# Kernel tuning notes

Hardware: AMD Instinct MI355X
Metric: run time of the kernel (lower is better)

The kernel has to match this reference:

```python
import jax, jax.numpy as jnp
import numpy as np

N_NODES = 150018  # n_users + n_items + n_genres
LATENT_DIM = 64
N_LAYERS = 3
N_EDGES = 4_800_000


def setup_inputs() -> dict:
    key = jax.random.key(0)
    k1, k2, k3, k4 = jax.random.split(key, 4)
    embedding = jax.random.normal(k1, (N_NODES, LATENT_DIM), dtype=jnp.float32) * 0.01
    vals = jax.random.uniform(k2, (N_EDGES,), dtype=jnp.float32)
    rows = jax.random.randint(k3, (N_EDGES,), 0, N_NODES, dtype=jnp.int32)
    cols = jax.random.randint(k4, (N_EDGES,), 0, N_NODES, dtype=jnp.int32)
    return {"embedding": embedding, "vals": vals, "rows": rows, "cols": cols}


def _spmm(vals, rows, cols, x):
    # sparse.mm(adj, x): out[r] += vals[e] * x[cols[e]] for each edge e
    gathered = x[cols] * vals[:, None]  # [E, D]
    return jax.ops.segment_sum(gathered, rows, num_segments=N_NODES)


def reference(embedding, vals, rows, cols):
    # LightGCN-style propagation; dropout is identity in eval mode (training=False)
    emb = embedding
    acc = emb
    for _ in range(N_LAYERS):
        emb = _spmm(vals, rows, cols, emb)
        acc = acc + emb
    # mean over (n_layers + 1) stacked layer outputs
    return acc / jnp.asarray(N_LAYERS + 1, dtype=embedding.dtype)
```

## Files before the change

### kernel.cpp

```cpp
#include <hip/hip_runtime.h>

#define N_NODES 150018
#define DIMS 64
#define NELEM (N_NODES * DIMS)
#define NVEC4 (NELEM / 4)
#define NBKT ((N_NODES + 255) >> 8)
#define BCAP 9216
#define PADCAP 1792
#define BSTRIDE (BCAP + PADCAP)
#define CH 8192
#define EPP 8
#define VINV 6.10388817e-05f

__device__ __forceinline__ unsigned short f2bf(float f) {
    unsigned int u = __float_as_uint(f);
    u += 0x7FFFu + ((u >> 16) & 1u);
    return (unsigned short)(u >> 16);
}
__device__ __forceinline__ float bf2f(unsigned short h) {
    return __uint_as_float(((unsigned int)h) << 16);
}

__global__ void conv_bf16_k(const float4* __restrict__ src, ushort4* __restrict__ dst, int n4) {
    int i = blockIdx.x * blockDim.x + threadIdx.x;
    if (i < n4) {
        float4 v = src[i];
        dst[i] = make_ushort4(f2bf(v.x), f2bf(v.y), f2bf(v.z), f2bf(v.w));
    }
}

__global__ void init_cursor_k(int* __restrict__ cursor) {
    int i = blockIdx.x * blockDim.x + threadIdx.x;
    if (i < NBKT) cursor[i] = i * BCAP;
}

__global__ __launch_bounds__(1024) void scatter_bucket_k(const int* __restrict__ rows,
                                 const int* __restrict__ cols,
                                 const float* __restrict__ vals, int* __restrict__ cursor,
                                 int2* __restrict__ edges1, int n) {
    __shared__ int2 staged[CH];
    __shared__ int cnt[NBKT];
    __shared__ int base[NBKT];
    __shared__ int lofs[NBKT];
    __shared__ int s[1024];
    const int t = threadIdx.x;
    const int beg = blockIdx.x * CH;
    const int end = min(n, beg + CH);
    const int cn = end - beg;

    for (int i = t; i < NBKT; i += 1024) cnt[i] = 0;
    __syncthreads();

    int er[EPP], ec[EPP];
    float ev[EPP];
    #pragma unroll
    for (int k = 0; k < EPP; ++k) {
        int e = beg + t + (k << 10);
        if (e < end) {
            er[k] = rows[e]; ec[k] = cols[e]; ev[k] = vals[e];
            atomicAdd(&cnt[er[k] >> 8], 1);
        } else er[k] = -1;
    }
    __syncthreads();

    for (int i = t; i < NBKT; i += 1024) {
        int c = cnt[i];
        base[i] = c ? atomicAdd(&cursor[i], c) : 0;
    }
    int v = (t < NBKT) ? cnt[t] : 0;
    s[t] = v;
    __syncthreads();
    for (int off = 1; off < 1024; off <<= 1) {
        int tv = (t >= off) ? s[t - off] : 0;
        __syncthreads();
        s[t] += tv;
        __syncthreads();
    }
    if (t < NBKT) { lofs[t] = s[t] - v; cnt[t] = 0; }
    __syncthreads();

    #pragma unroll
    for (int k = 0; k < EPP; ++k) {
        if (er[k] >= 0) {
            int b = er[k] >> 8;
            int p = lofs[b] + atomicAdd(&cnt[b], 1);
            unsigned int q = (unsigned int)(ev[k] * 16383.0f + 0.5f);
            staged[p] = make_int2(ec[k] | ((er[k] & 255) << 18),
                                  (int)(q | ((unsigned int)b << 14)));
        }
    }
    __syncthreads();

    for (int i = t; i < cn; i += 1024) {
        int2 st = staged[i];
        int b = ((unsigned int)st.y) >> 14;
        int gpos = base[b] + i - lofs[b];
        edges1[gpos] = make_int2(st.x, st.y & 0x3FFF);
    }
}

__global__ __launch_bounds__(512) void sort_bucket_k(const int2* __restrict__ e1,
                                 const int* __restrict__ bucket_end,
                                 unsigned int* __restrict__ e2,
                                 int* __restrict__ row_offs) {
    __shared__ int cnt[256];
    __shared__ int pref[256];
    __shared__ int rank[256];
    int b = blockIdx.x;
    int beg = b * BCAP, end = bucket_end[b];
    int padbase = b * BSTRIDE;
    if (threadIdx.x < 256) cnt[threadIdx.x] = 0;
    __syncthreads();
    for (int e = beg + threadIdx.x; e < end; e += 512)
        atomicAdd(&cnt[e1[e].x >> 18], 1);
    __syncthreads();
    int pc = 0;
    if (threadIdx.x < 256) {
        pc = (cnt[threadIdx.x] + 7) & ~7;
        pref[threadIdx.x] = pc;
    }
    __syncthreads();
    for (int off = 1; off < 256; off <<= 1) {
        int t = (threadIdx.x >= off && threadIdx.x < 256) ? pref[threadIdx.x - off] : 0;
        __syncthreads();
        if (threadIdx.x < 256) pref[threadIdx.x] += t;
        __syncthreads();
    }
    if (threadIdx.x < 256) {
        int ex = pref[threadIdx.x] - pc;
        row_offs[b * 257 + threadIdx.x] = padbase + ex;
        if (threadIdx.x == 255) row_offs[b * 257 + 256] = padbase + pref[255];
        pref[threadIdx.x] = ex;
        rank[threadIdx.x] = 0;
        int fb = padbase + ex + cnt[threadIdx.x];
        int fe = padbase + ex + pc;
        for (int i = fb; i < fe; ++i) e2[i] = 0u;
    }
    __syncthreads();
    for (int e = beg + threadIdx.x; e < end; e += 512) {
        int2 ed = e1[e];
        int slot = ed.x >> 18;
        int pos = padbase + pref[slot] + atomicAdd(&rank[slot], 1);
        e2[pos] = (unsigned int)(ed.x & 0x3FFFF) | (((unsigned int)ed.y) << 18);
    }
}

__global__ __launch_bounds__(256) void spmm_mid_k(const ushort4* __restrict__ xb,
                          const unsigned int* __restrict__ edges,
                          const int* __restrict__ row_offs,
                          ushort4* __restrict__ buf_out, int n_rows) {
    int row = (blockIdx.x * blockDim.x + threadIdx.x) >> 6;
    if (row >= n_rows) return;
    int lane = threadIdx.x & 63;
    int g = lane >> 4, q = lane & 15;
    int oi = (row >> 8) * 257 + (row & 255);
    int beg = row_offs[oi], end = row_offs[oi + 1];
    float4 a0 = make_float4(0.f, 0.f, 0.f, 0.f);
    float4 a1 = make_float4(0.f, 0.f, 0.f, 0.f);
    for (int e = beg; e < end; e += 8) {
        unsigned int w0 = edges[e + g];
        unsigned int w1 = edges[e + g + 4];
        ushort4 x0 = xb[((w0 & 0x3FFFFu) << 4) + q];
        ushort4 x1 = xb[((w1 & 0x3FFFFu) << 4) + q];
        float v0 = (float)(w0 >> 18) * VINV;
        float v1 = (float)(w1 >> 18) * VINV;
        a0.x = fmaf(v0, bf2f(x0.x), a0.x);  a0.y = fmaf(v0, bf2f(x0.y), a0.y);
        a0.z = fmaf(v0, bf2f(x0.z), a0.z);  a0.w = fmaf(v0, bf2f(x0.w), a0.w);
        a1.x = fmaf(v1, bf2f(x1.x), a1.x);  a1.y = fmaf(v1, bf2f(x1.y), a1.y);
        a1.z = fmaf(v1, bf2f(x1.z), a1.z);  a1.w = fmaf(v1, bf2f(x1.w), a1.w);
    }
    float4 a = make_float4(a0.x + a1.x, a0.y + a1.y, a0.z + a1.z, a0.w + a1.w);
    #pragma unroll
    for (int m = 16; m <= 32; m <<= 1) {
        a.x += __shfl_xor(a.x, m, 64);
        a.y += __shfl_xor(a.y, m, 64);
        a.z += __shfl_xor(a.z, m, 64);
        a.w += __shfl_xor(a.w, m, 64);
    }
    if (g == 0)
        buf_out[(row << 4) + q] = make_ushort4(f2bf(a.x), f2bf(a.y), f2bf(a.z), f2bf(a.w));
}

__global__ __launch_bounds__(256) void spmm_final_k(const ushort4* __restrict__ xb,
                          const unsigned int* __restrict__ edges,
                          const int* __restrict__ row_offs,
                          const ushort4* __restrict__ embb,
                          const ushort4* __restrict__ bufA,
                          const ushort4* __restrict__ bufB,
                          float4* __restrict__ out, int n_rows) {
    int row = (blockIdx.x * blockDim.x + threadIdx.x) >> 6;
    if (row >= n_rows) return;
    int lane = threadIdx.x & 63;
    int g = lane >> 4, q = lane & 15;
    int o = (row << 4) + q;

    ushort4 em = make_ushort4(0, 0, 0, 0);
    ushort4 ra = make_ushort4(0, 0, 0, 0), rb = make_ushort4(0, 0, 0, 0);
    if (g == 1) { em = embb[o]; ra = bufA[o]; rb = bufB[o]; }

    int oi = (row >> 8) * 257 + (row & 255);
    int beg = row_offs[oi], end = row_offs[oi + 1];
    float4 a0 = make_float4(0.f, 0.f, 0.f, 0.f);
    float4 a1 = make_float4(0.f, 0.f, 0.f, 0.f);
    for (int e = beg; e < end; e += 8) {
        unsigned int w0 = edges[e + g];
        unsigned int w1 = edges[e + g + 4];
        ushort4 x0 = xb[((w0 & 0x3FFFFu) << 4) + q];
        ushort4 x1 = xb[((w1 & 0x3FFFFu) << 4) + q];
        float v0 = (float)(w0 >> 18) * VINV;
        float v1 = (float)(w1 >> 18) * VINV;
        a0.x = fmaf(v0, bf2f(x0.x), a0.x);  a0.y = fmaf(v0, bf2f(x0.y), a0.y);
        a0.z = fmaf(v0, bf2f(x0.z), a0.z);  a0.w = fmaf(v0, bf2f(x0.w), a0.w);
        a1.x = fmaf(v1, bf2f(x1.x), a1.x);  a1.y = fmaf(v1, bf2f(x1.y), a1.y);
        a1.z = fmaf(v1, bf2f(x1.z), a1.z);  a1.w = fmaf(v1, bf2f(x1.w), a1.w);
    }
    float4 a = make_float4(a0.x + a1.x, a0.y + a1.y, a0.z + a1.z, a0.w + a1.w);
    #pragma unroll
    for (int m = 16; m <= 32; m <<= 1) {
        a.x += __shfl_xor(a.x, m, 64);
        a.y += __shfl_xor(a.y, m, 64);
        a.z += __shfl_xor(a.z, m, 64);
        a.w += __shfl_xor(a.w, m, 64);
    }
    if (g == 1) {
        float4 r;
        r.x = (bf2f(em.x) + bf2f(ra.x) + bf2f(rb.x) + a.x) * 0.25f;
        r.y = (bf2f(em.y) + bf2f(ra.y) + bf2f(rb.y) + a.y) * 0.25f;
        r.z = (bf2f(em.z) + bf2f(ra.z) + bf2f(rb.z) + a.z) * 0.25f;
        r.w = (bf2f(em.w) + bf2f(ra.w) + bf2f(rb.w) + a.w) * 0.25f;
        out[o] = r;
    }
}

extern "C" void kernel_launch(void* const* d_in, const int* in_sizes, int n_in,
                              void* d_out, int out_size, void* d_ws, size_t ws_size,
                              hipStream_t stream) {
    const float* emb  = (const float*)d_in[0];
    const float* vals = (const float*)d_in[1];
    const int*   rows = (const int*)d_in[2];
    const int*   cols = (const int*)d_in[3];
    float*       out  = (float*)d_out;
    const int n_edges = in_sizes[1];

    char* w = (char*)d_ws;
    int2*   edges1 = (int2*)w;
    ushort* bufAb  = (ushort*)w;
    ushort* bufBb  = (ushort*)(w + (size_t)NELEM * 2);
    w += (size_t)NBKT * BCAP * 8;
    unsigned int* edges2 = (unsigned int*)w;
    w += (size_t)NBKT * BSTRIDE * 4;
    ushort* embb   = (ushort*)w; w += (size_t)NELEM * 2;
    int* cursor    = (int*)w;    w += (size_t)NBKT * 4;
    int* row_offs  = (int*)w;

    const int scb = (n_edges + CH - 1) / CH;

    init_cursor_k<<<1, 1024, 0, stream>>>(cursor);
    scatter_bucket_k<<<scb, 1024, 0, stream>>>(rows, cols, vals, cursor, edges1, n_edges);
    sort_bucket_k<<<NBKT, 512, 0, stream>>>(edges1, cursor, edges2, row_offs);
    conv_bf16_k<<<(NVEC4 + 255) / 256, 256, 0, stream>>>((const float4*)emb,
                                                         (ushort4*)embb, NVEC4);

    const int sp_grid = (N_NODES + 3) / 4;
    spmm_mid_k<<<sp_grid, 256, 0, stream>>>((const ushort4*)embb, edges2, row_offs,
                                            (ushort4*)bufAb, N_NODES);
    spmm_mid_k<<<sp_grid, 256, 0, stream>>>((const ushort4*)bufAb, edges2, row_offs,
                                            (ushort4*)bufBb, N_NODES);
    spmm_final_k<<<sp_grid, 256, 0, stream>>>((const ushort4*)bufBb, edges2, row_offs,
                                              (const ushort4*)embb, (const ushort4*)bufAb,
                                              (const ushort4*)bufBb, (float4*)out, N_NODES);
}
```

Baseline: 378.3 us.

## Sub-sort edges within each row by column bin and stage bucket in LDS

The bucket sort now keys each edge on its row slot plus a 16-way column bin, so edges inside a row are grouped by column range. The intent is better cache locality for the x[col] gathers in the SpMM kernels. The bucket's edges are also staged in shared memory (about 74KB for the staged array and 32KB for the counters), so the second pass no longer rereads them from global memory. The larger LDS footprint lowers occupancy of the sort kernel, and the extra counting adds work there.

```diff
diff --git a/kernel.cpp b/kernel.cpp
--- a/kernel.cpp
+++ b/kernel.cpp
@@ -103,20 +103,29 @@
                                  const int* __restrict__ bucket_end,
                                  unsigned int* __restrict__ e2,
                                  int* __restrict__ row_offs) {
-    __shared__ int cnt[256];
+    __shared__ int2 staged[BCAP];
+    __shared__ int cnt[4096];
+    __shared__ int binoff[4096];
     __shared__ int pref[256];
-    __shared__ int rank[256];
     int b = blockIdx.x;
     int beg = b * BCAP, end = bucket_end[b];
+    int n = end - beg;
     int padbase = b * BSTRIDE;
-    if (threadIdx.x < 256) cnt[threadIdx.x] = 0;
-    __syncthreads();
-    for (int e = beg + threadIdx.x; e < end; e += 512)
-        atomicAdd(&cnt[e1[e].x >> 18], 1);
-    __syncthreads();
-    int pc = 0;
+    for (int i = threadIdx.x; i < 4096; i += 512) cnt[i] = 0;
+    __syncthreads();
+    for (int i = threadIdx.x; i < n; i += 512) {
+        int2 ed = e1[beg + i];
+        staged[i] = ed;
+        int slot = ed.x >> 18;
+        int colbin = (ed.x & 0x3FFFF) >> 14;
+        atomicAdd(&cnt[(slot << 4) | colbin], 1);
+    }
+    __syncthreads();
+    int tot = 0, pc = 0;
     if (threadIdx.x < 256) {
-        pc = (cnt[threadIdx.x] + 7) & ~7;
+        #pragma unroll
+        for (int j = 0; j < 16; ++j) tot += cnt[(threadIdx.x << 4) | j];
+        pc = (tot + 7) & ~7;
         pref[threadIdx.x] = pc;
     }
     __syncthreads();
@@ -130,18 +139,27 @@
         int ex = pref[threadIdx.x] - pc;
         row_offs[b * 257 + threadIdx.x] = padbase + ex;
         if (threadIdx.x == 255) row_offs[b * 257 + 256] = padbase + pref[255];
-        pref[threadIdx.x] = ex;
-        rank[threadIdx.x] = 0;
-        int fb = padbase + ex + cnt[threadIdx.x];
+        int off = ex;
+        #pragma unroll
+        for (int j = 0; j < 16; ++j) {
+            int key = (threadIdx.x << 4) | j;
+            binoff[key] = off;
+            off += cnt[key];
+        }
+        int fb = padbase + ex + tot;
         int fe = padbase + ex + pc;
         for (int i = fb; i < fe; ++i) e2[i] = 0u;
     }
     __syncthreads();
-    for (int e = beg + threadIdx.x; e < end; e += 512) {
-        int2 ed = e1[e];
+    for (int i = threadIdx.x; i < 4096; i += 512) cnt[i] = 0;
+    __syncthreads();
+    for (int i = threadIdx.x; i < n; i += 512) {
+        int2 ed = staged[i];
         int slot = ed.x >> 18;
-        int pos = padbase + pref[slot] + atomicAdd(&rank[slot], 1);
-        e2[pos] = (unsigned int)(ed.x & 0x3FFFF) | (((unsigned int)ed.y) << 18);
+        int col = ed.x & 0x3FFFF;
+        int key = (slot << 4) | (col >> 14);
+        int pos = padbase + binoff[key] + atomicAdd(&cnt[key], 1);
+        e2[pos] = (unsigned int)col | (((unsigned int)ed.y) << 18);
     }
 }
 
```

New measurement: 374.9 us. Within noise of the previous version (-0.9%).
